# Optimization experiments

Hardware: AMD Instinct MI355X
Metric: run time of the kernel (lower is better)

## Reference

```python
import jax, jax.numpy as jnp
import numpy as np

B, T, DIM, H = 2, 2048, 1024, 16
HD = DIM // H  # head_dim = 64
ROPE_BASE = 10000.0


def setup_inputs() -> dict:
    key = jax.random.key(0)
    k1, k2, k3, k4 = jax.random.split(key, 4)
    s = 1.0 / np.sqrt(DIM)
    return {
        "x": jax.random.normal(k1, (B, T, DIM), dtype=jnp.float32),
        "Wqkv": jax.random.normal(k2, (DIM, 3 * DIM), dtype=jnp.float32) * s,
        "Wout": jax.random.normal(k3, (DIM, DIM), dtype=jnp.float32) * s,
        "bout": jax.random.normal(k4, (DIM,), dtype=jnp.float32) * 0.01,
    }


def _rotate_half(x):
    # interleaved rotation: (x0,x1,x2,x3,...) -> (-x1,x0,-x3,x2,...)
    x1 = x[..., ::2]
    x2 = x[..., 1::2]
    return jnp.stack((-x2, x1), axis=-1).reshape(x.shape)


def _rope_cos_sin(seq_len, dtype):
    inv_freq = 1.0 / (ROPE_BASE ** (jnp.arange(0, HD, 2, dtype=jnp.float32) / HD))
    t = jnp.arange(seq_len, dtype=jnp.float32)
    freqs = t[:, None] * inv_freq[None, :]          # [T, HD/2]
    emb = jnp.concatenate((freqs, freqs), axis=-1)  # [T, HD] (cat layout, as in source)
    return jnp.cos(emb).astype(dtype), jnp.sin(emb).astype(dtype)


def reference(x, Wqkv, Wout, bout):
    b, t, _ = x.shape
    qkv = x @ Wqkv                                  # [B, T, 3*DIM]
    q, k, v = jnp.split(qkv, 3, axis=-1)
    # b t (h d) -> b h t d
    reshape = lambda z: z.reshape(b, t, H, HD).transpose(0, 2, 1, 3)
    q, k, v = reshape(q), reshape(k), reshape(v)
    cos, sin = _rope_cos_sin(t, x.dtype)            # [T, HD]
    q = q * cos + _rotate_half(q) * sin
    k = k * cos + _rotate_half(k) * sin
    scale = HD ** -0.5
    scores = jnp.einsum("bhqd,bhkd->bhqk", q, k) * scale
    attn = jax.nn.softmax(scores, axis=-1)
    out = jnp.einsum("bhqk,bhkd->bhqd", attn, v)    # [B, H, T, HD]
    out = out.transpose(0, 2, 1, 3).reshape(b, t, DIM)
    return out @ Wout + bout
```

## Files before the change

kernel.cpp:

```cpp
#include <hip/hip_runtime.h>
#include <math.h>


typedef unsigned short u16;
typedef __attribute__((ext_vector_type(8))) short short8;
typedef __attribute__((ext_vector_type(4))) short short4v;
typedef __attribute__((ext_vector_type(4))) float f32x4;
typedef __attribute__((ext_vector_type(16))) float f32x16;

#define T_SEQ 2048

#if __has_builtin(__builtin_amdgcn_exp2f)
#define EXP2(x) __builtin_amdgcn_exp2f(x)
#else
#define EXP2(x) exp2f(x)
#endif

__device__ __forceinline__ float b2f(u16 u) {
    union { unsigned int i; float f; } x; x.i = ((unsigned int)u) << 16; return x.f;
}
__device__ __forceinline__ u16 f2b(float f) {
    union { float f; unsigned int i; } x; x.f = f;
    return (u16)((x.i + 0x7FFFu + ((x.i >> 16) & 1u)) >> 16);
}
__device__ __forceinline__ void gl_lds16(const u16* g, u16* l) {
    __builtin_amdgcn_global_load_lds(
        (const __attribute__((address_space(1))) unsigned int*)g,
        (__attribute__((address_space(3))) unsigned int*)l, 16, 0, 0);
}
__device__ __forceinline__ short4v pack4(float a, float b, float c, float d) {
    union { float f; unsigned int u; } xa, xb, xc, xd;
    xa.f = a; xb.f = b; xc.f = c; xd.f = d;
    union { unsigned int u2[2]; short4v s; } r;
    r.u2[0] = (xa.u >> 16) | (xb.u & 0xffff0000u);
    r.u2[1] = (xc.u >> 16) | (xd.u & 0xffff0000u);
    return r.s;
}

__global__ __launch_bounds__(256) void setup_kernel(
    const float* __restrict__ x, const float* __restrict__ Wqkv,
    const float* __restrict__ Wout, u16* __restrict__ xb,
    u16* __restrict__ WqkvT, u16* __restrict__ WoutT,
    float* __restrict__ costab, float* __restrict__ sintab)
{
    const int bid = blockIdx.x;
    const int tid = threadIdx.x;

    if (bid < 4096) {
        int i = (bid * 256 + tid) * 4;
        float4 v = *(const float4*)(x + i);
        ushort4 w;
        w.x = f2b(v.x); w.y = f2b(v.y); w.z = f2b(v.z); w.w = f2b(v.w);
        *(ushort4*)(xb + i) = w;
        return;
    }
    if (bid < 8192) {
        const float* in; u16* out; int R, Cn, bx, by;
        if (bid < 7168) { in = Wqkv; out = WqkvT; R = 1024; Cn = 3072;
                          int id = bid - 4096; bx = id % 96; by = id / 96; }
        else            { in = Wout; out = WoutT; R = 1024; Cn = 1024;
                          int id = bid - 7168; bx = id & 31; by = id >> 5; }
        __shared__ u16 tile[32][33];
        const int tx = tid & 31, ty = tid >> 5;
        const int r0 = by * 32, c0 = bx * 32;
#pragma unroll
        for (int rr = ty; rr < 32; rr += 8)
            tile[tx][rr] = f2b(in[(size_t)(r0 + rr) * Cn + c0 + tx]);
        __syncthreads();
#pragma unroll
        for (int rr = ty; rr < 32; rr += 8)
            out[(size_t)(c0 + rr) * R + r0 + tx] = tile[rr][tx];
        return;
    }
    {
        int idx = (bid - 8192) * 256 + tid;
        int t = idx >> 6, d = idx & 63;
        const float nl32 = -0.28782313662425576f;
        float f = __expf((float)(d & 31) * nl32);
        float s, c;
        __sincosf((float)t * f, &s, &c);
        costab[idx] = c; sintab[idx] = s;
    }
}

template<int OBF>
__global__ __launch_bounds__(256) void gemm_bt_mfma(
    const u16* __restrict__ A, const u16* __restrict__ Bt,
    void* __restrict__ Cv, const float* __restrict__ bias,
    int M, int N, int K)
{
    __shared__ u16 As[128 * 32];
    __shared__ u16 Bs[128 * 32];

    const int tid = threadIdx.x;
    const int wave = tid >> 6, lane = tid & 63;
    const int col = lane & 15, quad = lane >> 4;
    const int wm = (wave & 1) * 64, wn = (wave >> 1) * 64;
    const int m0 = blockIdx.y * 128, n0 = blockIdx.x * 128;

    f32x4 acc[4][4];
#pragma unroll
    for (int i = 0; i < 4; ++i)
#pragma unroll
        for (int j = 0; j < 4; ++j) acc[i][j] = f32x4{0.f, 0.f, 0.f, 0.f};

    const int c1 = tid, c2 = tid + 256;
    const u16* a1 = A + (size_t)(m0 + (c1 >> 2)) * K + (c1 & 3) * 8;
    const u16* a2 = A + (size_t)(m0 + (c2 >> 2)) * K + (c2 & 3) * 8;
    const u16* b1 = Bt + (size_t)(n0 + (c1 >> 2)) * K + (c1 & 3) * 8;
    const u16* b2 = Bt + (size_t)(n0 + (c2 >> 2)) * K + (c2 & 3) * 8;
    u16* la1 = As + c1 * 8; u16* la2 = As + c2 * 8;
    u16* lb1 = Bs + c1 * 8; u16* lb2 = Bs + c2 * 8;

    for (int k0 = 0; k0 < K; k0 += 32) {
        __syncthreads();
        gl_lds16(a1 + k0, la1);
        gl_lds16(a2 + k0, la2);
        gl_lds16(b1 + k0, lb1);
        gl_lds16(b2 + k0, lb2);
        __syncthreads();

        short8 af[4], bfr[4];
#pragma unroll
        for (int i = 0; i < 4; ++i) {
            af[i]  = *(const short8*)&As[(wm + i * 16 + col) * 32 + quad * 8];
            bfr[i] = *(const short8*)&Bs[(wn + i * 16 + col) * 32 + quad * 8];
        }
#pragma unroll
        for (int i = 0; i < 4; ++i)
#pragma unroll
            for (int j = 0; j < 4; ++j)
                acc[i][j] = __builtin_amdgcn_mfma_f32_16x16x32_bf16(
                    af[i], bfr[j], acc[i][j], 0, 0, 0);
    }

#pragma unroll
    for (int j = 0; j < 4; ++j) {
        int n = n0 + wn + j * 16 + col;
        float bv = bias ? bias[n] : 0.f;
#pragma unroll
        for (int i = 0; i < 4; ++i) {
            int mbase = m0 + wm + i * 16 + quad * 4;
#pragma unroll
            for (int r = 0; r < 4; ++r) {
                if (OBF) ((u16*)Cv)[(size_t)(mbase + r) * N + n] = f2b(acc[i][j][r] + bv);
                else     ((float*)Cv)[(size_t)(mbase + r) * N + n] = acc[i][j][r] + bv;
            }
        }
    }
}

__global__ __launch_bounds__(256) void prep_kernel(
    const u16* __restrict__ qkvb, const float* __restrict__ costab,
    const float* __restrict__ sintab, u16* __restrict__ Qb,
    u16* __restrict__ Kb, u16* __restrict__ Vimg)
{
    __shared__ u16 Vls[64][72];

    const int tid = threadIdx.x;
    const int bh = blockIdx.y;
    const int t0 = blockIdx.x * 64;
    const int b = bh >> 4, h = bh & 15;
    const int t_loc = tid >> 2;
    const int d0 = (tid & 3) * 16;

    const int t = t0 + t_loc;
    const u16* qp = qkvb + ((size_t)(b * T_SEQ + t)) * 3072 + h * 64 + d0;

    float ct[16], st[16];
    {
        const float* cp = costab + (size_t)t * 64 + d0;
        const float* sp = sintab + (size_t)t * 64 + d0;
#pragma unroll
        for (int j = 0; j < 16; j += 4) {
            *(float4*)&ct[j] = *(const float4*)(cp + j);
            *(float4*)&st[j] = *(const float4*)(sp + j);
        }
    }

#pragma unroll
    for (int part = 0; part < 2; ++part) {
        const float sc = part ? 1.f : 0.18033688011112042f;
        const u16* src = qp + part * 1024;
        u16* dst = (part ? Kb : Qb) + ((size_t)(bh * T_SEQ + t)) * 64 + d0;
        short8 v0 = *(const short8*)(src);
        short8 v1 = *(const short8*)(src + 8);
        float f[16];
#pragma unroll
        for (int j = 0; j < 8; ++j) { f[j] = b2f((u16)v0[j]); f[8 + j] = b2f((u16)v1[j]); }
        u16 o[16];
#pragma unroll
        for (int i = 0; i < 8; ++i) {
            float e = f[2 * i], od = f[2 * i + 1];
            o[2 * i]     = f2b((e * ct[2 * i]      - od * st[2 * i]) * sc);
            o[2 * i + 1] = f2b((od * ct[2 * i + 1] + e  * st[2 * i + 1]) * sc);
        }
        *(short8*)(dst)     = *(short8*)&o[0];
        *(short8*)(dst + 8) = *(short8*)&o[8];
    }

    {
        const u16* src = qp + 2048;
        *(short8*)&Vls[t_loc][d0]     = *(const short8*)(src);
        *(short8*)&Vls[t_loc][d0 + 8] = *(const short8*)(src + 8);
    }
    __syncthreads();
    {
        const int dt    = tid >> 7;
        const int g     = (tid >> 5) & 3;
        const int hi2   = (tid >> 4) & 1;
        const int dpair = tid & 15;
        const int kl0 = g * 8 + hi2 * 4;
        const int d0v = dt * 32 + 2 * dpair;
        const int kt_base = blockIdx.x * 2;
#pragma unroll
        for (int ktl = 0; ktl < 2; ++ktl) {
            u16 o[8];
#pragma unroll
            for (int j = 0; j < 4; ++j) {
                o[j]     = Vls[ktl * 32 + kl0 + j][d0v];
                o[4 + j] = Vls[ktl * 32 + kl0 + j][d0v + 1];
            }
            u16* dst = Vimg + ((size_t)(bh * 64 + kt_base + ktl)) * 2048 + tid * 8;
            *(short8*)dst = *(short8*)&o[0];
        }
    }
}

__global__ __launch_bounds__(256, 2) void attn32_kernel(
    const u16* __restrict__ Qb, const u16* __restrict__ Kb,
    const u16* __restrict__ Vimg, float* __restrict__ po, float* __restrict__ pl)
{
    __shared__ u16 Kbuf[2][2][2048];
    __shared__ u16 Vbuf[2][2][2048];

    const int tid = threadIdx.x;
    const int wave = tid >> 6, lane = tid & 63;
    const int qcol = lane & 31;
    const int hi = lane >> 5;

    const int bid = blockIdx.x;
    const int lbid = (bid & 7) * 64 + (bid >> 3);
    const int bh = lbid >> 4;
    const int seg = (lbid >> 3) & 1;
    const int qblk = lbid & 7;
    const int qrow0 = qblk * 256 + wave * 64;

    short8 qa[2][4];
#pragma unroll
    for (int qs = 0; qs < 2; ++qs) {
        const u16* qp = Qb + ((size_t)(bh * T_SEQ + qrow0 + qs * 32 + qcol)) * 64 + hi * 8;
#pragma unroll
        for (int c = 0; c < 4; ++c) qa[qs][c] = *(const short8*)(qp + c * 16);
    }

    f32x16 O00, O01, O10, O11;
#pragma unroll
    for (int i = 0; i < 16; ++i) { O00[i] = 0.f; O01[i] = 0.f; O10[i] = 0.f; O11[i] = 0.f; }
    float Lacc0 = 0.f, Lacc1 = 0.f;

    const u16* kg_ptr = Kb + ((size_t)bh * T_SEQ + qcol) * 64 + wave * 16 + hi * 8;
    const u16* vg_ptr = Vimg + ((size_t)bh * 64) * 2048 + tid * 8;

    const int kt0 = seg * 32;

    gl_lds16(kg_ptr + (size_t)kt0 * 2048,       &Kbuf[0][0][tid * 8]);
    gl_lds16(kg_ptr + (size_t)(kt0 + 1) * 2048, &Kbuf[0][1][tid * 8]);
    gl_lds16(vg_ptr + (size_t)kt0 * 2048,       &Vbuf[0][0][tid * 8]);
    gl_lds16(vg_ptr + (size_t)(kt0 + 1) * 2048, &Vbuf[0][1][tid * 8]);
    __syncthreads();

    for (int r = 0; r < 16; ++r) {
        const int cur = r & 1;

        short8 kf[2][4];
        short4v vv[2][8];
#pragma unroll
        for (int half = 0; half < 2; ++half) {
#pragma unroll
            for (int f = 0; f < 4; ++f)
                kf[half][f] = *(const short8*)&Kbuf[cur][half][(f * 64 + lane) * 8];
#pragma unroll
            for (int g = 0; g < 4; ++g) {
                vv[half][2 * g]     = *(const short4v*)&Vbuf[cur][half][g * 256 + lane * 4];
                vv[half][2 * g + 1] = *(const short4v*)&Vbuf[cur][half][1024 + g * 256 + lane * 4];
            }
        }

        if (r < 15) {
            const int kt = kt0 + (r + 1) * 2;
            gl_lds16(kg_ptr + (size_t)kt * 2048,       &Kbuf[cur ^ 1][0][tid * 8]);
            gl_lds16(kg_ptr + (size_t)(kt + 1) * 2048, &Kbuf[cur ^ 1][1][tid * 8]);
            gl_lds16(vg_ptr + (size_t)kt * 2048,       &Vbuf[cur ^ 1][0][tid * 8]);
            gl_lds16(vg_ptr + (size_t)(kt + 1) * 2048, &Vbuf[cur ^ 1][1][tid * 8]);
        }

#pragma unroll
        for (int half = 0; half < 2; ++half) {
            f32x16 sT0, sT1;
#pragma unroll
            for (int ii = 0; ii < 16; ++ii) { sT0[ii] = 0.f; sT1[ii] = 0.f; }
#pragma unroll
            for (int c = 0; c < 4; ++c) {
                sT0 = __builtin_amdgcn_mfma_f32_32x32x16_bf16(kf[half][c], qa[0][c], sT0, 0, 0, 0);
                sT1 = __builtin_amdgcn_mfma_f32_32x32x16_bf16(kf[half][c], qa[1][c], sT1, 0, 0, 0);
            }

            {
                float pe[16];
#pragma unroll
                for (int ii = 0; ii < 16; ++ii) pe[ii] = EXP2(sT0[ii]);
                short4v pb[4];
#pragma unroll
                for (int g = 0; g < 4; ++g) {
                    pb[g] = pack4(pe[4 * g + 0], pe[4 * g + 1],
                                  pe[4 * g + 2], pe[4 * g + 3]);
                    Lacc0 += (pe[4 * g + 0] + pe[4 * g + 1]) +
                             (pe[4 * g + 2] + pe[4 * g + 3]);
                }
#pragma unroll
                for (int g = 0; g < 4; ++g) {
                    O00 = __builtin_amdgcn_mfma_f32_32x32x8bf16_1k(vv[half][2 * g],     pb[g], O00, 0, 0, 0);
                    O01 = __builtin_amdgcn_mfma_f32_32x32x8bf16_1k(vv[half][2 * g + 1], pb[g], O01, 0, 0, 0);
                }
            }
            {
                float pe[16];
#pragma unroll
                for (int ii = 0; ii < 16; ++ii) pe[ii] = EXP2(sT1[ii]);
                short4v pb[4];
#pragma unroll
                for (int g = 0; g < 4; ++g) {
                    pb[g] = pack4(pe[4 * g + 0], pe[4 * g + 1],
                                  pe[4 * g + 2], pe[4 * g + 3]);
                    Lacc1 += (pe[4 * g + 0] + pe[4 * g + 1]) +
                             (pe[4 * g + 2] + pe[4 * g + 3]);
                }
#pragma unroll
                for (int g = 0; g < 4; ++g) {
                    O10 = __builtin_amdgcn_mfma_f32_32x32x8bf16_1k(vv[half][2 * g],     pb[g], O10, 0, 0, 0);
                    O11 = __builtin_amdgcn_mfma_f32_32x32x8bf16_1k(vv[half][2 * g + 1], pb[g], O11, 0, 0, 0);
                }
            }
        }

        __syncthreads();
    }

    float Lq0 = Lacc0 + __shfl(Lacc0, lane ^ 32);
    float Lq1 = Lacc1 + __shfl(Lacc1, lane ^ 32);

    const size_t prow0 = ((size_t)(seg * 32 + bh)) * T_SEQ + qrow0 + qcol;
    const size_t prow1 = prow0 + 32;
    float* op0 = po + prow0 * 64;
    float* op1 = po + prow1 * 64;
#pragma unroll
    for (int g2 = 0; g2 < 4; ++g2) {
        int dd = g2 * 8 + hi * 4;
        *(float4*)(op0 + dd)      = make_float4(O00[4 * g2 + 0], O00[4 * g2 + 1],
                                                O00[4 * g2 + 2], O00[4 * g2 + 3]);
        *(float4*)(op0 + 32 + dd) = make_float4(O01[4 * g2 + 0], O01[4 * g2 + 1],
                                                O01[4 * g2 + 2], O01[4 * g2 + 3]);
        *(float4*)(op1 + dd)      = make_float4(O10[4 * g2 + 0], O10[4 * g2 + 1],
                                                O10[4 * g2 + 2], O10[4 * g2 + 3]);
        *(float4*)(op1 + 32 + dd) = make_float4(O11[4 * g2 + 0], O11[4 * g2 + 1],
                                                O11[4 * g2 + 2], O11[4 * g2 + 3]);
    }
    if (hi == 0) { pl[prow0] = Lq0; pl[prow1] = Lq1; }
}

__global__ __launch_bounds__(256) void attn_combine_kernel(
    const float* __restrict__ po, const float* __restrict__ pl,
    u16* __restrict__ aob)
{
    const int idx = blockIdx.x * 256 + (int)threadIdx.x;
    const int row = idx >> 4;
    const int d4 = idx & 15;

    float4 o0 = *(const float4*)(po + (size_t)row * 64 + d4 * 4);
    float4 o1 = *(const float4*)(po + ((size_t)row + 65536) * 64 + d4 * 4);
    float L = pl[row] + pl[row + 65536];
    float inv = 1.f / L;

    const int bh = row >> 11, t = row & 2047;
    const int b = bh >> 4, h = bh & 15;
    ushort4 w;
    w.x = f2b((o0.x + o1.x) * inv);
    w.y = f2b((o0.y + o1.y) * inv);
    w.z = f2b((o0.z + o1.z) * inv);
    w.w = f2b((o0.w + o1.w) * inv);
    *(ushort4*)(aob + ((size_t)(b * T_SEQ + t)) * 1024 + h * 64 + d4 * 4) = w;
}

extern "C" void kernel_launch(void* const* d_in, const int* in_sizes, int n_in,
                              void* d_out, int out_size, void* d_ws, size_t ws_size,
                              hipStream_t stream)
{
    const float* x    = (const float*)d_in[0];
    const float* Wqkv = (const float*)d_in[1];
    const float* Wout = (const float*)d_in[2];
    const float* bout = (const float*)d_in[3];
    float* out = (float*)d_out;

    char* w = (char*)d_ws;
    u16* qkvb    = (u16*)(w);
    u16* xb      = (u16*)(w + 25165824);
    u16* WqkvT   = (u16*)(w + 33554432);
    u16* WoutT   = (u16*)(w + 39845888);
    u16* aob     = (u16*)(w + 41943040);
    u16* Qb      = (u16*)(w + 50331648);
    u16* Kb      = (u16*)(w + 58720256);
    u16* Vimg    = (u16*)(w + 67108864);
    float* ctab  = (float*)(w + 75497472);
    float* stab  = (float*)(w + 76021760);
    float* po    = (float*)(w);
    float* pl    = (float*)(w + 33554432);

    dim3 blk(256);
    setup_kernel<<<dim3(8704), blk, 0, stream>>>(x, Wqkv, Wout, xb, WqkvT, WoutT, ctab, stab);
    gemm_bt_mfma<1><<<dim3(24, 32), blk, 0, stream>>>(xb, WqkvT, qkvb, nullptr, 4096, 3072, 1024);
    prep_kernel<<<dim3(32, 32), blk, 0, stream>>>(qkvb, ctab, stab, Qb, Kb, Vimg);
    attn32_kernel<<<dim3(512), blk, 0, stream>>>(Qb, Kb, Vimg, po, pl);
    attn_combine_kernel<<<dim3(4096), blk, 0, stream>>>(po, pl, aob);
    gemm_bt_mfma<0><<<dim3(8, 32), blk, 0, stream>>>(aob, WoutT, out, bout, 4096, 1024, 1024);
}
```

Before: 211.7 us.

## Triple-buffer K/V LDS loads with partial vmcnt waits and MFMA priority

Moves the attention kernel's K/V staging from double to triple buffering, so two tiles are in flight while a third is being computed. The full __syncthreads at the end of each iteration becomes a partial s_waitcnt vmcnt plus s_barrier at the start. s_setprio is raised around the MFMA blocks so matrix work gets issue priority over other waves. LDS use per block grows from 32KB to 48KB, which may lower occupancy under launch_bounds(256,2). The hand-written waitcnt also relies on the compiler's exact load count.

```diff
diff --git a/kernel.cpp b/kernel.cpp
--- a/kernel.cpp
+++ b/kernel.cpp
@@ -231,8 +231,8 @@
     const u16* __restrict__ Qb, const u16* __restrict__ Kb,
     const u16* __restrict__ Vimg, float* __restrict__ po, float* __restrict__ pl)
 {
-    __shared__ u16 Kbuf[2][2][2048];
-    __shared__ u16 Vbuf[2][2][2048];
+    __shared__ u16 Kbuf[3][2][2048];
+    __shared__ u16 Vbuf[3][2][2048];
 
     const int tid = threadIdx.x;
     const int wave = tid >> 6, lane = tid & 63;
@@ -264,14 +264,24 @@
 
     const int kt0 = seg * 32;
 
-    gl_lds16(kg_ptr + (size_t)kt0 * 2048,       &Kbuf[0][0][tid * 8]);
-    gl_lds16(kg_ptr + (size_t)(kt0 + 1) * 2048, &Kbuf[0][1][tid * 8]);
-    gl_lds16(vg_ptr + (size_t)kt0 * 2048,       &Vbuf[0][0][tid * 8]);
-    gl_lds16(vg_ptr + (size_t)(kt0 + 1) * 2048, &Vbuf[0][1][tid * 8]);
-    __syncthreads();
-
+#define STAGE(p, rr) do {                                                     \
+        const int kt_ = kt0 + (rr) * 2;                                       \
+        gl_lds16(kg_ptr + (size_t)kt_ * 2048,       &Kbuf[p][0][tid * 8]);    \
+        gl_lds16(kg_ptr + (size_t)(kt_ + 1) * 2048, &Kbuf[p][1][tid * 8]);    \
+        gl_lds16(vg_ptr + (size_t)kt_ * 2048,       &Vbuf[p][0][tid * 8]);    \
+        gl_lds16(vg_ptr + (size_t)(kt_ + 1) * 2048, &Vbuf[p][1][tid * 8]);    \
+    } while (0)
+
+    STAGE(0, 0);
+    STAGE(1, 1);
+
+    int cur = 0, prv = 2;
     for (int r = 0; r < 16; ++r) {
-        const int cur = r & 1;
+        if (r < 15) asm volatile("s_waitcnt vmcnt(4)" ::: "memory");
+        else        asm volatile("s_waitcnt vmcnt(0)" ::: "memory");
+        __builtin_amdgcn_s_barrier();
+        asm volatile("" ::: "memory");
+        __builtin_amdgcn_sched_barrier(0);
 
         short8 kf[2][4];
         short4v vv[2][8];
@@ -287,24 +297,20 @@
             }
         }
 
-        if (r < 15) {
-            const int kt = kt0 + (r + 1) * 2;
-            gl_lds16(kg_ptr + (size_t)kt * 2048,       &Kbuf[cur ^ 1][0][tid * 8]);
-            gl_lds16(kg_ptr + (size_t)(kt + 1) * 2048, &Kbuf[cur ^ 1][1][tid * 8]);
-            gl_lds16(vg_ptr + (size_t)kt * 2048,       &Vbuf[cur ^ 1][0][tid * 8]);
-            gl_lds16(vg_ptr + (size_t)(kt + 1) * 2048, &Vbuf[cur ^ 1][1][tid * 8]);
-        }
+        if (r < 14) STAGE(prv, r + 2);
 
 #pragma unroll
         for (int half = 0; half < 2; ++half) {
             f32x16 sT0, sT1;
 #pragma unroll
             for (int ii = 0; ii < 16; ++ii) { sT0[ii] = 0.f; sT1[ii] = 0.f; }
+            __builtin_amdgcn_s_setprio(1);
 #pragma unroll
             for (int c = 0; c < 4; ++c) {
                 sT0 = __builtin_amdgcn_mfma_f32_32x32x16_bf16(kf[half][c], qa[0][c], sT0, 0, 0, 0);
                 sT1 = __builtin_amdgcn_mfma_f32_32x32x16_bf16(kf[half][c], qa[1][c], sT1, 0, 0, 0);
             }
+            __builtin_amdgcn_s_setprio(0);
 
             {
                 float pe[16];
@@ -318,11 +324,13 @@
                     Lacc0 += (pe[4 * g + 0] + pe[4 * g + 1]) +
                              (pe[4 * g + 2] + pe[4 * g + 3]);
                 }
+                __builtin_amdgcn_s_setprio(1);
 #pragma unroll
                 for (int g = 0; g < 4; ++g) {
                     O00 = __builtin_amdgcn_mfma_f32_32x32x8bf16_1k(vv[half][2 * g],     pb[g], O00, 0, 0, 0);
                     O01 = __builtin_amdgcn_mfma_f32_32x32x8bf16_1k(vv[half][2 * g + 1], pb[g], O01, 0, 0, 0);
                 }
+                __builtin_amdgcn_s_setprio(0);
             }
             {
                 float pe[16];
@@ -336,16 +344,20 @@
                     Lacc1 += (pe[4 * g + 0] + pe[4 * g + 1]) +
                              (pe[4 * g + 2] + pe[4 * g + 3]);
                 }
+                __builtin_amdgcn_s_setprio(1);
 #pragma unroll
                 for (int g = 0; g < 4; ++g) {
                     O10 = __builtin_amdgcn_mfma_f32_32x32x8bf16_1k(vv[half][2 * g],     pb[g], O10, 0, 0, 0);
                     O11 = __builtin_amdgcn_mfma_f32_32x32x8bf16_1k(vv[half][2 * g + 1], pb[g], O11, 0, 0, 0);
                 }
-            }
-        }
-
-        __syncthreads();
-    }
+                __builtin_amdgcn_s_setprio(0);
+            }
+        }
+
+        prv = cur;
+        cur = (cur == 2) ? 0 : cur + 1;
+    }
+#undef STAGE
 
     float Lq0 = Lacc0 + __shfl(Lacc0, lane ^ 32);
     float Lq1 = Lacc1 + __shfl(Lacc1, lane ^ 32);
```

Result: no change. 208.4 us (-1.5%).
